# Performance work log

Measured on AMD Instinct MI355X. Metric: run time of the kernel, lower is better.

## Reference

```python
import jax, jax.numpy as jnp
import numpy as np

N, E, EL = 100000, 1600000, 200000
IN_FEATS, H, N_LAYERS = 128, 128, 3
HL = ((N_LAYERS + 1) * H) // 2  # PyG JK-LSTM hidden = (num_layers*channels)//2 = 256
EPS = 1e-5


def setup_inputs() -> dict:
    key = jax.random.key(0)
    ks = jax.random.split(key, 16)
    p = lambda k, shape: (jax.random.normal(k, shape, jnp.float32) * 0.05)
    return {
        "edge_index": jax.random.randint(ks[0], (2, E), 0, N),
        "x": jax.random.normal(ks[1], (N, IN_FEATS), jnp.float32),
        "edge_label_index": jax.random.randint(ks[2], (2, EL), 0, N),
        # GCNConv
        "gcn_w": p(ks[3], (IN_FEATS, H)), "gcn_b": jnp.zeros((H,), jnp.float32),
        # SGConv stack (lin applied AFTER propagation, K=1)
        "sg_w": p(ks[4], (N_LAYERS, H, H)), "sg_b": jnp.zeros((N_LAYERS, H), jnp.float32),
        # shared BatchNorm used between conv layers
        "bn_gamma": jnp.ones((H,), jnp.float32), "bn_beta": jnp.zeros((H,), jnp.float32),
        # bidirectional LSTM for JumpingKnowledge (torch gate order i,f,g,o)
        "w_ih_f": p(ks[5], (4 * HL, H)), "w_hh_f": p(ks[6], (4 * HL, HL)),
        "b_ih_f": jnp.zeros((4 * HL,), jnp.float32), "b_hh_f": jnp.zeros((4 * HL,), jnp.float32),
        "w_ih_b": p(ks[7], (4 * HL, H)), "w_hh_b": p(ks[8], (4 * HL, HL)),
        "b_ih_b": jnp.zeros((4 * HL,), jnp.float32), "b_hh_b": jnp.zeros((4 * HL,), jnp.float32),
        "att_w": p(ks[9], (2 * HL, 1)), "att_b": jnp.zeros((1,), jnp.float32),
        # edge predictor MLP
        "pred1_w": p(ks[10], (2 * H, H)), "pred1_b": jnp.zeros((H,), jnp.float32),
        "pbn_gamma": jnp.ones((H,), jnp.float32), "pbn_beta": jnp.zeros((H,), jnp.float32),
        "pred2_w": p(ks[11], (H, 1)), "pred2_b": jnp.zeros((1,), jnp.float32),
    }


def gcn_prop(x, src, dst, n):
    deg = jnp.zeros((n,), x.dtype).at[dst].add(jnp.ones((src.shape[0],), x.dtype)) + 1.0
    dinv = jax.lax.rsqrt(deg)
    norm = dinv[src] * dinv[dst]  # [E]
    out = jnp.zeros_like(x).at[dst].add(norm[:, None] * x[src])
    return out + (dinv * dinv)[:, None] * x  # self-loop contribution


def batchnorm(h, g, b):
    mu = h.mean(axis=0)
    var = ((h - mu) ** 2).mean(axis=0)
    return (h - mu) * jax.lax.rsqrt(var + EPS) * g + b


def lstm_dir(xs, w_ih, w_hh, b_ih, b_hh):
    # xs: [L, N, C] -> hidden states [L, N, HL]
    n = xs.shape[1]
    hh = w_hh.shape[1]
    def step(carry, xt):
        h, c = carry
        gates = xt @ w_ih.T + h @ w_hh.T + b_ih + b_hh
        i, f, g, o = jnp.split(gates, 4, axis=-1)
        c = jax.nn.sigmoid(f) * c + jax.nn.sigmoid(i) * jnp.tanh(g)
        h = jax.nn.sigmoid(o) * jnp.tanh(c)
        return (h, c), h
    init = (jnp.zeros((n, hh), xs.dtype), jnp.zeros((n, hh), xs.dtype))
    _, hs = jax.lax.scan(step, init, xs)
    return hs


def reference(edge_index, x, edge_label_index, gcn_w, gcn_b, sg_w, sg_b,
              bn_gamma, bn_beta, w_ih_f, w_hh_f, b_ih_f, b_hh_f,
              w_ih_b, w_hh_b, b_ih_b, b_hh_b, att_w, att_b,
              pred1_w, pred1_b, pbn_gamma, pbn_beta, pred2_w, pred2_b):
    src, dst = edge_index[0], edge_index[1]
    n = x.shape[0]
    hs = []
    # GCNConv: linear transform, then normalized propagation, then bias
    h = gcn_prop(x @ gcn_w, src, dst, n) + gcn_b
    h = batchnorm(jax.nn.relu(h), bn_gamma, bn_beta)  # dropout = identity (eval)
    hs.append(h)
    # SGConv (K=1): propagate then linear; last layer has no act/norm
    for i in range(N_LAYERS):
        h = gcn_prop(h, src, dst, n) @ sg_w[i] + sg_b[i]
        if i < N_LAYERS - 1:
            h = batchnorm(jax.nn.relu(h), bn_gamma, bn_beta)
        hs.append(h)
    xs = jnp.stack(hs, axis=0)  # [L, N, H]
    hf = lstm_dir(xs, w_ih_f, w_hh_f, b_ih_f, b_hh_f)
    hb = lstm_dir(xs[::-1], w_ih_b, w_hh_b, b_ih_b, b_hh_b)[::-1]
    seq = jnp.concatenate([hf, hb], axis=-1)  # [L, N, 2*HL]
    alpha = jax.nn.softmax((seq @ att_w)[..., 0] + att_b[0], axis=0)  # softmax over layers
    jk = jnp.einsum('lnh,ln->nh', xs, alpha)  # [N, H]
    # edge-level predictor
    row, col = edge_label_index[0], edge_label_index[1]
    z = jnp.concatenate([jk[row], jk[col]], axis=-1)  # [EL, 2H]
    z = jax.nn.relu(z @ pred1_w + pred1_b)
    z = batchnorm(z, pbn_gamma, pbn_beta)  # dropout = identity (eval)
    z = z @ pred2_w + pred2_b
    return jax.nn.sigmoid(z)
```

## Files before the change

### kernel.cpp

```cpp
#include <hip/hip_runtime.h>
#include <cstdint>

#define CDIV(a,b) (((a)+(b)-1)/(b))

typedef __bf16 bf16x8 __attribute__((ext_vector_type(8)));
typedef float  f32x4  __attribute__((ext_vector_type(4)));

__device__ __forceinline__ float bf2f(unsigned short u) {
    unsigned v = ((unsigned)u) << 16;
    float f; __builtin_memcpy(&f, &v, 4); return f;
}
__device__ __forceinline__ unsigned short f2bf(float f) {
    unsigned u; __builtin_memcpy(&u, &f, 4);
    u += 0x7fffu + ((u >> 16) & 1u);
    return (unsigned short)(u >> 16);
}
__device__ __forceinline__ float fsig(float x) { return 1.f / (1.f + __expf(-x)); }
__device__ __forceinline__ float ftanh(float x) { return 2.f * fsig(2.f * x) - 1.f; }

__device__ __forceinline__ void gld_lds16(const void* g, void* l) {
    __builtin_amdgcn_global_load_lds((__attribute__((address_space(1))) void*)(g),
                                     (__attribute__((address_space(3))) void*)(l), 16, 0, 0);
}


__global__ __launch_bounds__(256) void k_zero4(uint4* p, size_t n4) {
    size_t i = (size_t)blockIdx.x * 256 + threadIdx.x;
    if (i < n4) p[i] = make_uint4(0, 0, 0, 0);
}

__global__ __launch_bounds__(256) void k_deg(const int* ei, int* degi, int E) {
    int e = blockIdx.x * 256 + threadIdx.x;
    if (e < E) atomicAdd(&degi[ei[E + e]], 1);
}

__global__ __launch_bounds__(256) void k_dinv(const int* degi, float* dinv, int N) {
    int n = blockIdx.x * 256 + threadIdx.x;
    if (n < N) dinv[n] = rsqrtf((float)degi[n] + 1.f);
}

#define SCAN_B 2048
__global__ __launch_bounds__(256) void k_scan1(const int* in, int* out, int* bsum, int n) {
    __shared__ int ls[256];
    int b = blockIdx.x, t = threadIdx.x;
    int base = b * SCAN_B + t * 8;
    int v[8]; int s = 0;
#pragma unroll
    for (int i = 0; i < 8; ++i) { int idx = base + i; v[i] = (idx < n) ? in[idx] : 0; s += v[i]; }
    ls[t] = s; __syncthreads();
    for (int off = 1; off < 256; off <<= 1) {
        int x = (t >= off) ? ls[t - off] : 0;
        __syncthreads();
        ls[t] += x;
        __syncthreads();
    }
    int ex = ls[t] - s;
    if (t == 255) bsum[b] = ls[255];
    int run = ex;
#pragma unroll
    for (int i = 0; i < 8; ++i) { int idx = base + i; if (idx < n) out[idx] = run; run += v[i]; }
}
__global__ void k_scan2(int* bsum, int nb) {
    if (threadIdx.x == 0) {
        int acc = 0;
        for (int b = 0; b < nb; ++b) { int v = bsum[b]; bsum[b] = acc; acc += v; }
    }
}
__global__ __launch_bounds__(256) void k_scan3(int* rowp, int* curs, const int* bsum, int n) {
    int i = blockIdx.x * 256 + threadIdx.x;
    if (i < n) { int v = rowp[i] + bsum[i / SCAN_B]; rowp[i] = v; curs[i] = v; }
}
__global__ __launch_bounds__(256) void k_fill(const int* ei, int* curs, int* csr, int E) {
    int e = blockIdx.x * 256 + threadIdx.x;
    if (e < E) { int d = ei[E + e]; int pos = atomicAdd(&curs[d], 1); csr[pos] = ei[e]; }
}

__global__ __launch_bounds__(256) void k_xconv(const float* x, unsigned short* xb, int N, int Npad) {
    int idx = blockIdx.x * 256 + threadIdx.x;
    if (idx >= Npad * 64) return;
    int n = idx >> 6, q = idx & 63;
    ushort2 o;
    if (n < N) {
        float2 v = *(const float2*)&x[(size_t)n * 128 + q * 2];
        o = make_ushort2(f2bf(v.x), f2bf(v.y));
    } else o = make_ushort2(0, 0);
    *(ushort2*)&xb[(size_t)n * 128 + q * 2] = o;
}

__global__ __launch_bounds__(256) void k_packT(const float* W, unsigned short* BT, int K, int Nout) {
    int idx = blockIdx.x * 256 + threadIdx.x;
    if (idx >= K * Nout) return;
    int o = idx / K, k = idx % K;
    BT[idx] = f2bf(W[(size_t)k * Nout + o]);
}

__global__ __launch_bounds__(256) void k_packlstm4(const float* wih, const float* whh, unsigned short* BT) {
    int idx = blockIdx.x * 256 + threadIdx.x;
    if (idx >= 1024 * 384) return;
    int e = idx & 7, u = idx >> 3;
    int l4 = u & 3, l15 = (u >> 2) & 15, ni = (u >> 6) & 1;
    int rest = u >> 7;
    int ks = rest % 12, G = rest / 12;
    int gate = ni * 2 + (l15 >> 3);
    int hid = G * 8 + (l15 & 7);
    int srow = gate * 256 + hid;
    int k = ks * 32 + l4 * 8 + e;
    float v = (k < 128) ? wih[(size_t)srow * 128 + k] : whh[(size_t)srow * 256 + (k - 128)];
    BT[idx] = f2bf(v);
}
__global__ __launch_bounds__(256) void k_packbias4(const float* bih, const float* bhh, float* bias) {
    int c = blockIdx.x * 256 + threadIdx.x;
    if (c >= 1024) return;
    int G = c >> 5, cc = c & 31;
    int ni = cc >> 4, ll = cc & 15;
    int gate = ni * 2 + (ll >> 3);
    int hid = G * 8 + (ll & 7);
    int srow = gate * 256 + hid;
    bias[c] = bih[srow] + bhh[srow];
}


__global__ __launch_bounds__(256) void k_prop(const unsigned short* __restrict__ X,
                                              const int* __restrict__ rowp, const int* __restrict__ cnt,
                                              const int* __restrict__ csr, const float* __restrict__ dinv,
                                              const float* __restrict__ bias, int relu,
                                              int N, int Npad, unsigned short* __restrict__ OUT) {
    int node = (blockIdx.x * 256 + threadIdx.x) >> 4;
    if (node >= Npad) return;
    const int g = threadIdx.x & 15;
    unsigned short* op = OUT + (size_t)node * 128 + g * 8;
    if (node >= N) { *(uint4*)op = make_uint4(0, 0, 0, 0); return; }
    const int beg = rowp[node], num = cnt[node];
    const float di = dinv[node];
    float a[8];
#pragma unroll
    for (int j = 0; j < 8; ++j) a[j] = 0.f;
    if (num > 0) {
        int s = csr[beg];
        float ws = dinv[s];
        uint4 q = *(const uint4*)&X[(size_t)s * 128 + g * 8];
        for (int i = 0; i < num; ++i) {
            int sn = (i + 1 < num) ? csr[beg + i + 1] : s;
            float wn = dinv[sn];
            uint4 qn = *(const uint4*)&X[(size_t)sn * 128 + g * 8];
            unsigned q0 = q.x, q1 = q.y, q2 = q.z, q3 = q.w;
            a[0] = fmaf(ws, bf2f((unsigned short)(q0 & 0xffffu)), a[0]);
            a[1] = fmaf(ws, bf2f((unsigned short)(q0 >> 16)), a[1]);
            a[2] = fmaf(ws, bf2f((unsigned short)(q1 & 0xffffu)), a[2]);
            a[3] = fmaf(ws, bf2f((unsigned short)(q1 >> 16)), a[3]);
            a[4] = fmaf(ws, bf2f((unsigned short)(q2 & 0xffffu)), a[4]);
            a[5] = fmaf(ws, bf2f((unsigned short)(q2 >> 16)), a[5]);
            a[6] = fmaf(ws, bf2f((unsigned short)(q3 & 0xffffu)), a[6]);
            a[7] = fmaf(ws, bf2f((unsigned short)(q3 >> 16)), a[7]);
            s = sn; ws = wn; q = qn;
        }
    }
    uint4 xq = *(const uint4*)&X[(size_t)node * 128 + g * 8];
    unsigned x0 = xq.x, x1 = xq.y, x2 = xq.z, x3 = xq.w;
    const float dd = di * di;
    float o0 = di * a[0] + dd * bf2f((unsigned short)(x0 & 0xffffu));
    float o1 = di * a[1] + dd * bf2f((unsigned short)(x0 >> 16));
    float o2 = di * a[2] + dd * bf2f((unsigned short)(x1 & 0xffffu));
    float o3 = di * a[3] + dd * bf2f((unsigned short)(x1 >> 16));
    float o4 = di * a[4] + dd * bf2f((unsigned short)(x2 & 0xffffu));
    float o5 = di * a[5] + dd * bf2f((unsigned short)(x2 >> 16));
    float o6 = di * a[6] + dd * bf2f((unsigned short)(x3 & 0xffffu));
    float o7 = di * a[7] + dd * bf2f((unsigned short)(x3 >> 16));
    if (bias) {
        const float* bp = bias + g * 8;
        o0 += bp[0]; o1 += bp[1]; o2 += bp[2]; o3 += bp[3];
        o4 += bp[4]; o5 += bp[5]; o6 += bp[6]; o7 += bp[7];
    }
    if (relu) {
        o0 = fmaxf(o0, 0.f); o1 = fmaxf(o1, 0.f); o2 = fmaxf(o2, 0.f); o3 = fmaxf(o3, 0.f);
        o4 = fmaxf(o4, 0.f); o5 = fmaxf(o5, 0.f); o6 = fmaxf(o6, 0.f); o7 = fmaxf(o7, 0.f);
    }
    uint4 r;
    r.x = (unsigned)f2bf(o0) | ((unsigned)f2bf(o1) << 16);
    r.y = (unsigned)f2bf(o2) | ((unsigned)f2bf(o3) << 16);
    r.z = (unsigned)f2bf(o4) | ((unsigned)f2bf(o5) << 16);
    r.w = (unsigned)f2bf(o6) | ((unsigned)f2bf(o7) << 16);
    *(uint4*)op = r;
}


__global__ __launch_bounds__(256) void k_stats(const unsigned short* __restrict__ X, int rows, float* part) {
    __shared__ float ls[512];
    int t = threadIdx.x, b = blockIdx.x;
    int ch = t & 127, half = t >> 7;
    float s = 0.f, s2 = 0.f;
    for (int r = b * 2 + half; r < rows; r += 512) {
        float v = bf2f(X[(size_t)r * 128 + ch]);
        s += v; s2 += v * v;
    }
    ls[t] = s; ls[256 + t] = s2;
    __syncthreads();
    if (t < 128) {
        part[b * 256 + t] = ls[t] + ls[t + 128];
        part[b * 256 + 128 + t] = ls[256 + t] + ls[256 + t + 128];
    }
}
__global__ void k_bnfinal(const float* part, int nb, float rows,
                          const float* gamma, const float* beta, float* bnst) {
    int ch = threadIdx.x;
    if (ch >= 128) return;
    float s = 0.f, s2 = 0.f;
    for (int b = 0; b < nb; ++b) { s += part[b * 256 + ch]; s2 += part[b * 256 + 128 + ch]; }
    float mu = s / rows, var = s2 / rows - mu * mu;
    float sc = gamma[ch] * rsqrtf(var + 1e-5f);
    bnst[ch] = sc;
    bnst[128 + ch] = beta[ch] - mu * sc;
}
__global__ __launch_bounds__(256) void k_apply(const unsigned short* in, const float* bnst,
                                               unsigned short* outv, int N, int Npad) {
    int idx = blockIdx.x * 256 + threadIdx.x;
    if (idx >= Npad * 64) return;
    int n = idx >> 6, q = idx & 63;
    ushort2 o;
    if (n < N) {
        ushort2 v = *(const ushort2*)&in[(size_t)n * 128 + q * 2];
        int c0 = q * 2;
        o = make_ushort2(f2bf(bf2f(v.x) * bnst[c0] + bnst[128 + c0]),
                         f2bf(bf2f(v.y) * bnst[c0 + 1] + bnst[128 + c0 + 1]));
    } else o = make_ushort2(0, 0);
    *(ushort2*)&outv[(size_t)n * 128 + q * 2] = o;
}


template<int GATHER>
__device__ __forceinline__ void gemm_core(
    const unsigned short* __restrict__ A0, int lda0, int K0,
    const unsigned short* __restrict__ A1, int lda1, int Ktot,
    const unsigned short* __restrict__ BT, int ldb,
    const int* __restrict__ gR, const int* __restrict__ gC, int ELr,
    int m0, int c0, unsigned short* sA, unsigned short* sB, f32x4 acc[4][4]) {
    const int tid = threadIdx.x;
    const int wid = tid >> 6, lane = tid & 63;
    const int l15 = lane & 15, l4 = lane >> 4;
    const int wr = (wid >> 1) * 64, wc = (wid & 1) * 64;
    const int crow = lane >> 3;
    const int cslot = (lane & 7) ^ crow;
    const int nK = Ktot >> 6;
    for (int ks = 0; ks < nK; ++ks) {
        const int k0 = ks << 6;
#pragma unroll
        for (int i = 0; i < 4; ++i) {
            const int chunk = wid * 4 + i;
            const int row = chunk * 8 + crow;
            const unsigned short* bs = BT + (size_t)(c0 + row) * ldb + k0 + (cslot << 3);
            gld_lds16(bs, sB + chunk * 512);
            if constexpr (GATHER) {
                int e = m0 + row; if (e >= ELr) e = ELr - 1;
                const int nid = (k0 < K0) ? gR[e] : gC[e];
                const unsigned short* as = A0 + (size_t)nid * lda0 + (k0 & (K0 - 1)) + (lane & 7) * 8;
                *(uint4*)(sA + chunk * 512 + crow * 64 + (((lane & 7) ^ crow) << 3)) = *(const uint4*)as;
            } else {
                const unsigned short* as = (k0 < K0)
                    ? A0 + (size_t)(m0 + row) * lda0 + k0 + (cslot << 3)
                    : A1 + (size_t)(m0 + row) * lda1 + (k0 - K0) + (cslot << 3);
                gld_lds16(as, sA + chunk * 512);
            }
        }
        __syncthreads();
#pragma unroll
        for (int kk = 0; kk < 2; ++kk) {
            const int c8 = kk * 4 + l4;
            const int rs = l15 & 7;
            bf16x8 av[4], bv[4];
#pragma unroll
            for (int i = 0; i < 4; ++i)
                av[i] = *(const bf16x8*)(sA + (wr + i * 16 + l15) * 64 + ((c8 ^ rs) << 3));
#pragma unroll
            for (int i = 0; i < 4; ++i)
                bv[i] = *(const bf16x8*)(sB + (wc + i * 16 + l15) * 64 + ((c8 ^ rs) << 3));
#pragma unroll
            for (int mi = 0; mi < 4; ++mi)
#pragma unroll
                for (int ni = 0; ni < 4; ++ni)
                    acc[mi][ni] = __builtin_amdgcn_mfma_f32_16x16x32_bf16(av[mi], bv[ni], acc[mi][ni], 0, 0, 0);
        }
        __syncthreads();
    }
}

template<int GATHER>
__global__ __launch_bounds__(256) void k_gemm(
    const unsigned short* __restrict__ A0, int lda0, int K0,
    const unsigned short* __restrict__ A1, int lda1, int Ktot,
    const unsigned short* __restrict__ BT, int ldb,
    const int* __restrict__ gR, const int* __restrict__ gC, int ELr,
    const float* __restrict__ bias, int relu,
    unsigned short* __restrict__ C, int ldc, int NT) {
    extern __shared__ char smem[];
    unsigned short* sA = (unsigned short*)smem;
    unsigned short* sB = (unsigned short*)(smem + 16384);
    int mt = blockIdx.x / NT, nt = blockIdx.x % NT;
    int m0 = mt * 128, c0 = nt * 128;
    f32x4 acc[4][4];
#pragma unroll
    for (int a = 0; a < 4; ++a)
#pragma unroll
        for (int b = 0; b < 4; ++b) acc[a][b] = (f32x4){0.f, 0.f, 0.f, 0.f};
    gemm_core<GATHER>(A0, lda0, K0, A1, lda1, Ktot, BT, ldb, gR, gC, ELr, m0, c0, sA, sB, acc);
    const int tid = threadIdx.x;
    const int wid = tid >> 6, lane = tid & 63;
    const int l15 = lane & 15, l4 = lane >> 4;
    const int wr = (wid >> 1) * 64, wc = (wid & 1) * 64;
#pragma unroll
    for (int ni = 0; ni < 4; ++ni) {
        int col = c0 + wc + ni * 16 + l15;
        float bv = bias ? bias[col] : 0.f;
#pragma unroll
        for (int mi = 0; mi < 4; ++mi) {
            int rbase = m0 + wr + mi * 16 + l4 * 4;
#pragma unroll
            for (int j = 0; j < 4; ++j) {
                float v = acc[mi][ni][j] + bv;
                if (relu) v = fmaxf(v, 0.f);
                C[(size_t)(rbase + j) * ldc + col] = f2bf(v);
            }
        }
    }
}


__global__ __launch_bounds__(1024)
void k_lstm_fused(
    const unsigned short* __restrict__ xs,
    const unsigned short* __restrict__ BT2f, const unsigned short* __restrict__ BT2b,
    const float* __restrict__ bias2f, const float* __restrict__ bias2b,
    const float* __restrict__ att_w,
    float* __restrict__ scores,
    int N, int Npad) {
    __shared__ unsigned short xls[64 * 128];
    __shared__ unsigned short hbuf[2][64 * 256];
    __shared__ float c_ld[64 * 256];
    __shared__ float sc_ld[16][64];

    const int tid = threadIdx.x;
    const int wid = tid >> 6, lane = tid & 63;
    const int l15 = lane & 15, l4 = lane >> 4;
    const int rs = l15 & 7;
    const int m0 = blockIdx.x * 64;
    const int loff = (l15 * 4 + l4) * 8;
    const bool hi = (l15 & 8) != 0;

    float scl[4] = {0.f, 0.f, 0.f, 0.f};

#pragma unroll 1
    for (int dir = 0; dir < 2; ++dir) {
        const unsigned short* BT2 = dir ? BT2b : BT2f;
        const float* bias2 = dir ? bias2b : bias2f;
        const float* attw = att_w + dir * 256;
        for (int i = tid; i < 2048; i += 1024) ((uint4*)hbuf[0])[i] = make_uint4(0, 0, 0, 0);
        for (int i = tid; i < 4096; i += 1024) ((uint4*)c_ld)[i] = make_uint4(0, 0, 0, 0);
        __syncthreads();
        unsigned short* hcur = hbuf[0];
        unsigned short* hnxt = hbuf[1];

#pragma unroll 1
        for (int t = 0; t < 4; ++t) {
            const int lyr = dir ? (3 - t) : t;
            if (wid < 8) {
                const unsigned short* xl = xs + (size_t)lyr * Npad * 128;
#pragma unroll
                for (int i = 0; i < 2; ++i) {
                    int chunk = wid * 2 + i;
                    int row = chunk * 4 + l4;
                    gld_lds16(xl + (size_t)(m0 + row) * 128 + ((l15 ^ (row & 7)) << 3),
                              xls + chunk * 512);
                }
            }
            __syncthreads();

            float scA[4], scB[4];
#pragma unroll
            for (int a = 0; a < 4; ++a) { scA[a] = 0.f; scB[a] = 0.f; }

#pragma unroll 1
            for (int p = 0; p < 2; ++p) {
                const int G = wid * 2 + p;
                f32x4 acc[4][2];
#pragma unroll
                for (int a = 0; a < 4; ++a) {
                    acc[a][0] = (f32x4){0.f, 0.f, 0.f, 0.f};
                    acc[a][1] = (f32x4){0.f, 0.f, 0.f, 0.f};
                }
                const unsigned short* bp = BT2 + (size_t)G * 12288 + loff;
                bf16x8 f0a = *(const bf16x8*)(bp);
                bf16x8 f0b = *(const bf16x8*)(bp + 512);
                bf16x8 f1a = *(const bf16x8*)(bp + 1024);
                bf16x8 f1b = *(const bf16x8*)(bp + 1536);
#pragma unroll 1
                for (int ks = 0; ks < 4; ++ks) {
                    bf16x8 bv0 = f0a, bv1 = f0b;
                    f0a = f1a; f0b = f1b;
                    f1a = *(const bf16x8*)(bp + ((ks + 2) * 2 + 0) * 512);
                    f1b = *(const bf16x8*)(bp + ((ks + 2) * 2 + 1) * 512);
#pragma unroll
                    for (int mi = 0; mi < 4; ++mi) {
                        bf16x8 av = *(const bf16x8*)(xls + (mi * 16 + l15) * 128 +
                                                     (((ks * 4 + l4) ^ rs) << 3));
                        acc[mi][0] = __builtin_amdgcn_mfma_f32_16x16x32_bf16(av, bv0, acc[mi][0], 0, 0, 0);
                        acc[mi][1] = __builtin_amdgcn_mfma_f32_16x16x32_bf16(av, bv1, acc[mi][1], 0, 0, 0);
                    }
                }
#pragma unroll 1
                for (int ks = 4; ks < 12; ++ks) {
                    bf16x8 bv0 = f0a, bv1 = f0b;
                    f0a = f1a; f0b = f1b;
                    f1a = *(const bf16x8*)(bp + ((ks + 2) * 2 + 0) * 512);
                    f1b = *(const bf16x8*)(bp + ((ks + 2) * 2 + 1) * 512);
#pragma unroll
                    for (int mi = 0; mi < 4; ++mi) {
                        bf16x8 av = *(const bf16x8*)(hcur + (mi * 16 + l15) * 256 +
                                                     ((((ks - 4) * 4 + l4) ^ rs) << 3));
                        acc[mi][0] = __builtin_amdgcn_mfma_f32_16x16x32_bf16(av, bv0, acc[mi][0], 0, 0, 0);
                        acc[mi][1] = __builtin_amdgcn_mfma_f32_16x16x32_bf16(av, bv1, acc[mi][1], 0, 0, 0);
                    }
                }
                const float bi0 = bias2[G * 32 + l15];
                const float bi1 = bias2[G * 32 + 16 + l15];
                const float aw = attw[G * 8 + (l15 & 7)];
#pragma unroll
                for (int mi = 0; mi < 4; ++mi) {
                    float a00 = acc[mi][0][0] + bi0, a01 = acc[mi][0][1] + bi0;
                    float a02 = acc[mi][0][2] + bi0, a03 = acc[mi][0][3] + bi0;
                    float a10 = acc[mi][1][0] + bi1, a11 = acc[mi][1][1] + bi1;
                    float a12 = acc[mi][1][2] + bi1, a13 = acc[mi][1][3] + bi1;
                    float r0 = __shfl_xor(hi ? a00 : a02, 8);
                    float r1 = __shfl_xor(hi ? a01 : a03, 8);
                    float r2 = __shfl_xor(hi ? a10 : a12, 8);
                    float r3 = __shfl_xor(hi ? a11 : a13, 8);
                    float iA = hi ? r0  : a00,  fA = hi ? a02 : r0;
                    float gA = hi ? r2  : a10,  oA = hi ? a12 : r2;
                    float iB = hi ? r1  : a01,  fB = hi ? a03 : r1;
                    float gB = hi ? r3  : a11,  oB = hi ? a13 : r3;
                    const int rA = mi * 16 + l4 * 4 + (hi ? 2 : 0);
                    {
                        float gi = fsig(iA), gf = fsig(fA), gg = ftanh(gA), go = fsig(oA);
                        const int ca = rA * 256 + (((G ^ ((rA >> 2) & 7)) << 3) + (l15 & 7));
                        float cc = fmaf(gf, c_ld[ca], gi * gg);
                        c_ld[ca] = cc;
                        float hn = go * ftanh(cc);
                        scA[mi] = fmaf(hn, aw, scA[mi]);
                        *(unsigned short*)((char*)hnxt + rA * 512 +
                                           ((G ^ (rA & 7)) << 4) + (l15 & 7) * 2) = f2bf(hn);
                    }
                    {
                        const int rB = rA + 1;
                        float gi = fsig(iB), gf = fsig(fB), gg = ftanh(gB), go = fsig(oB);
                        const int cb = rB * 256 + (((G ^ ((rB >> 2) & 7)) << 3) + (l15 & 7));
                        float cc = fmaf(gf, c_ld[cb], gi * gg);
                        c_ld[cb] = cc;
                        float hn = go * ftanh(cc);
                        scB[mi] = fmaf(hn, aw, scB[mi]);
                        *(unsigned short*)((char*)hnxt + rB * 512 +
                                           ((G ^ (rB & 7)) << 4) + (l15 & 7) * 2) = f2bf(hn);
                    }
                }
            }
#pragma unroll
            for (int mi = 0; mi < 4; ++mi) {
                float sA = scA[mi], sB = scB[mi];
                sA += __shfl_xor(sA, 1); sA += __shfl_xor(sA, 2); sA += __shfl_xor(sA, 4);
                sB += __shfl_xor(sB, 1); sB += __shfl_xor(sB, 2); sB += __shfl_xor(sB, 4);
                if ((l15 & 7) == 0) {
                    int row = mi * 16 + l4 * 4 + (hi ? 2 : 0);
                    sc_ld[wid][row] = sA;
                    sc_ld[wid][row + 1] = sB;
                }
            }
            __syncthreads();
            if (tid < 64) {
                float s = 0.f;
#pragma unroll
                for (int w = 0; w < 16; ++w) s += sc_ld[w][tid];
#pragma unroll
                for (int l = 0; l < 4; ++l) scl[l] += (l == lyr) ? s : 0.f;
            }
            unsigned short* tmp = hcur; hcur = hnxt; hnxt = tmp;
        }
    }
    if (tid < 64) {
        int n = m0 + tid;
        if (n < N) {
#pragma unroll
            for (int l = 0; l < 4; ++l) scores[(size_t)l * N + n] = scl[l];
        }
    }
}


__global__ __launch_bounds__(256) void k_jk(const float* __restrict__ sc, const unsigned short* __restrict__ xs,
                                            unsigned short* __restrict__ jk, int N, int Npad) {
    int gw = (blockIdx.x * 256 + threadIdx.x) >> 6;
    if (gw >= N) return;
    int lane = threadIdx.x & 63;
    float s0 = sc[gw], s1 = sc[N + gw], s2 = sc[2 * N + gw], s3 = sc[3 * N + gw];
    float m = fmaxf(fmaxf(s0, s1), fmaxf(s2, s3));
    float e0 = __expf(s0 - m), e1 = __expf(s1 - m), e2 = __expf(s2 - m), e3 = __expf(s3 - m);
    float inv = 1.f / (e0 + e1 + e2 + e3);
    float a0 = e0 * inv, a1 = e1 * inv, a2 = e2 * inv, a3 = e3 * inv;
    size_t stride = (size_t)Npad * 128;
    const unsigned short* p = xs + (size_t)gw * 128 + lane * 2;
    ushort2 v0 = *(const ushort2*)p;
    ushort2 v1 = *(const ushort2*)(p + stride);
    ushort2 v2 = *(const ushort2*)(p + 2 * stride);
    ushort2 v3 = *(const ushort2*)(p + 3 * stride);
    float r0 = a0 * bf2f(v0.x) + a1 * bf2f(v1.x) + a2 * bf2f(v2.x) + a3 * bf2f(v3.x);
    float r1 = a0 * bf2f(v0.y) + a1 * bf2f(v1.y) + a2 * bf2f(v2.y) + a3 * bf2f(v3.y);
    *(ushort2*)&jk[(size_t)gw * 128 + lane * 2] = make_ushort2(f2bf(r0), f2bf(r1));
}

__global__ __launch_bounds__(256) void k_final(const unsigned short* __restrict__ z1, const float* __restrict__ bnst,
                                               const float* __restrict__ w2, const float* __restrict__ b2,
                                               float* __restrict__ out, int EL) {
    int e = (blockIdx.x * 256 + threadIdx.x) >> 6;
    if (e >= EL) return;
    int lane = threadIdx.x & 63;
    ushort2 z = *(const ushort2*)&z1[(size_t)e * 128 + lane * 2];
    int c0 = lane * 2;
    float y0 = bf2f(z.x) * bnst[c0] + bnst[128 + c0];
    float y1 = bf2f(z.y) * bnst[c0 + 1] + bnst[128 + c0 + 1];
    float p = y0 * w2[c0] + y1 * w2[c0 + 1];
#pragma unroll
    for (int off = 32; off; off >>= 1) p += __shfl_xor(p, off);
    if (lane == 0) out[e] = 1.f / (1.f + __expf(-(p + b2[0])));
}


extern "C" void kernel_launch(void* const* d_in, const int* in_sizes, int n_in,
                              void* d_out, int out_size, void* d_ws, size_t ws_size,
                              hipStream_t stream) {
    const int* ei      = (const int*)d_in[0];
    const float* x     = (const float*)d_in[1];
    const int* eli     = (const int*)d_in[2];
    const float* gcn_w = (const float*)d_in[3];
    const float* gcn_b = (const float*)d_in[4];
    const float* sg_w  = (const float*)d_in[5];
    const float* sg_b  = (const float*)d_in[6];
    const float* bn_g  = (const float*)d_in[7];
    const float* bn_b  = (const float*)d_in[8];
    const float* w_ih_f = (const float*)d_in[9];
    const float* w_hh_f = (const float*)d_in[10];
    const float* b_ih_f = (const float*)d_in[11];
    const float* b_hh_f = (const float*)d_in[12];
    const float* w_ih_b = (const float*)d_in[13];
    const float* w_hh_b = (const float*)d_in[14];
    const float* b_ih_b = (const float*)d_in[15];
    const float* b_hh_b = (const float*)d_in[16];
    const float* att_w = (const float*)d_in[17];
    const float* p1_w  = (const float*)d_in[19];
    const float* p1_b  = (const float*)d_in[20];
    const float* pbn_g = (const float*)d_in[21];
    const float* pbn_b = (const float*)d_in[22];
    const float* p2_w  = (const float*)d_in[23];
    const float* p2_b  = (const float*)d_in[24];

    const int E = in_sizes[0] / 2;
    const int N = in_sizes[1] / 128;
    const int EL = in_sizes[2] / 2;
    const int Npad = CDIV(N, 128) * 128;
    const int ELpad = CDIV(EL, 128) * 128;
    const size_t NB128 = (size_t)Npad * 128 * 2;

    char* wsp = (char*)d_ws;
    size_t off = 0;
    auto A = [&](size_t b) -> char* {
        char* p = wsp + off;
        off = (off + b + 255) & ~(size_t)255;
        return p;
    };
    int* degi = (int*)A((size_t)N * 4);
    float* dinv = (float*)A((size_t)N * 4);
    int* rowp = (int*)A((size_t)N * 4);
    int* curs = (int*)A((size_t)N * 4);
    int* bsum = (int*)A(256 * 4);
    unsigned short* gT   = (unsigned short*)A(128 * 128 * 2);
    unsigned short* sgT  = (unsigned short*)A(3 * 128 * 128 * 2);
    unsigned short* p1T  = (unsigned short*)A(128 * 256 * 2);
    unsigned short* BTf  = (unsigned short*)A(1024 * 384 * 2);
    unsigned short* BTb  = (unsigned short*)A(1024 * 384 * 2);
    float* biasf = (float*)A(1024 * 4);
    float* biasb = (float*)A(1024 * 4);
    float* part = (float*)A(256 * 256 * 4);
    float* bnst = (float*)A(256 * 4);
    float* scores = (float*)A((size_t)4 * N * 4);
    unsigned short* xs = (unsigned short*)A(NB128 * 4);
    const size_t arena0 = off;
    int* csr = (int*)A((size_t)E * 4);
    unsigned short* xb   = (unsigned short*)A(NB128);
    unsigned short* bufA = (unsigned short*)A(NB128);
    unsigned short* bufB = (unsigned short*)A(NB128);
    const size_t convEnd = off;
    off = arena0;
    unsigned short* jk = (unsigned short*)A((size_t)N * 128 * 2);
    unsigned short* z1 = (unsigned short*)A((size_t)ELpad * 128 * 2);
    const size_t predEnd = off;
    if (convEnd > ws_size || predEnd > ws_size) return;

    k_zero4<<<CDIV((size_t)N * 4, 16 * 256), 256, 0, stream>>>((uint4*)degi, CDIV((size_t)N * 4, 16));
    k_deg<<<CDIV(E, 256), 256, 0, stream>>>(ei, degi, E);
    k_dinv<<<CDIV(N, 256), 256, 0, stream>>>(degi, dinv, N);
    int nb = CDIV(N, SCAN_B);
    k_scan1<<<nb, 256, 0, stream>>>(degi, rowp, bsum, N);
    k_scan2<<<1, 64, 0, stream>>>(bsum, nb);
    k_scan3<<<CDIV(N, 256), 256, 0, stream>>>(rowp, curs, bsum, N);
    k_fill<<<CDIV(E, 256), 256, 0, stream>>>(ei, curs, csr, E);

    k_xconv<<<CDIV(Npad * 64, 256), 256, 0, stream>>>(x, xb, N, Npad);
    k_packT<<<CDIV(128 * 128, 256), 256, 0, stream>>>(gcn_w, gT, 128, 128);
    for (int i = 0; i < 3; ++i)
        k_packT<<<CDIV(128 * 128, 256), 256, 0, stream>>>(sg_w + (size_t)i * 128 * 128, sgT + (size_t)i * 128 * 128, 128, 128);
    k_packT<<<CDIV(256 * 128, 256), 256, 0, stream>>>(p1_w, p1T, 256, 128);
    k_packlstm4<<<CDIV(1024 * 384, 256), 256, 0, stream>>>(w_ih_f, w_hh_f, BTf);
    k_packlstm4<<<CDIV(1024 * 384, 256), 256, 0, stream>>>(w_ih_b, w_hh_b, BTb);
    k_packbias4<<<4, 256, 0, stream>>>(b_ih_f, b_hh_f, biasf);
    k_packbias4<<<4, 256, 0, stream>>>(b_ih_b, b_hh_b, biasb);

    const int MT = Npad / 128;
    k_gemm<0><<<MT, 256, 32768, stream>>>(xb, 128, 128, nullptr, 0, 128, gT, 128,
                                          nullptr, nullptr, 0, nullptr, 0, bufA, 128, 1);
    k_prop<<<CDIV(Npad * 16, 256), 256, 0, stream>>>(bufA, rowp, degi, csr, dinv, gcn_b, 1, N, Npad, bufB);
    k_stats<<<256, 256, 0, stream>>>(bufB, N, part);
    k_bnfinal<<<1, 128, 0, stream>>>(part, 256, (float)N, bn_g, bn_b, bnst);
    k_apply<<<CDIV(Npad * 64, 256), 256, 0, stream>>>(bufB, bnst, xs, N, Npad);

    for (int i = 0; i < 3; ++i) {
        k_prop<<<CDIV(Npad * 16, 256), 256, 0, stream>>>(xs + (size_t)i * Npad * 128, rowp, degi, csr, dinv,
                                                         nullptr, 0, N, Npad, bufA);
        unsigned short* dst = (i < 2) ? bufB : xs + (size_t)3 * Npad * 128;
        k_gemm<0><<<MT, 256, 32768, stream>>>(bufA, 128, 128, nullptr, 0, 128,
                                              sgT + (size_t)i * 128 * 128, 128,
                                              nullptr, nullptr, 0, sg_b + i * 128, (i < 2) ? 1 : 0, dst, 128, 1);
        if (i < 2) {
            k_stats<<<256, 256, 0, stream>>>(bufB, N, part);
            k_bnfinal<<<1, 128, 0, stream>>>(part, 256, (float)N, bn_g, bn_b, bnst);
            k_apply<<<CDIV(Npad * 64, 256), 256, 0, stream>>>(bufB, bnst, xs + (size_t)(i + 1) * Npad * 128, N, Npad);
        }
    }

    k_lstm_fused<<<Npad / 64, 1024, 0, stream>>>(xs, BTf, BTb, biasf, biasb, att_w, scores, N, Npad);

    k_jk<<<CDIV(N * 64, 256), 256, 0, stream>>>(scores, xs, jk, N, Npad);

    const int MTe = ELpad / 128;
    k_gemm<1><<<MTe, 256, 32768, stream>>>(jk, 128, 128, nullptr, 0, 256, p1T, 256,
                                           eli, eli + EL, EL, p1_b, 1, z1, 128, 1);
    k_stats<<<256, 256, 0, stream>>>(z1, EL, part);
    k_bnfinal<<<1, 128, 0, stream>>>(part, 256, (float)EL, pbn_g, pbn_b, bnst);
    k_final<<<CDIV(EL * 64, 256), 256, 0, stream>>>(z1, bnst, p2_w, p2_b, (float*)d_out, EL);
    (void)n_in; (void)out_size;
}
```

Before: 2.546 ms.

## Keep LSTM cell state in registers and halve LSTM block to 512 threads

The fused LSTM kernel now runs 8 waves per block, each handling four gate groups instead of two, and keeps the cell state in per-thread registers rather than a 64KB shared-memory array. The score-reduction scratch is aliased onto the x tile buffer, so shared memory per block drops from about 112KB to about 80KB, which may let more blocks share a CU. The intent is to cut LDS traffic for the cell state and raise occupancy. In exchange each wave does twice the serial work, register pressure rises, the B-operand prefetch pipelining is removed, and an extra barrier is added per timestep.

```diff
diff --git a/kernel.cpp b/kernel.cpp
--- a/kernel.cpp
+++ b/kernel.cpp
@@ -324,7 +324,7 @@
 }
 
 
-__global__ __launch_bounds__(1024)
+__global__ __launch_bounds__(512)
 void k_lstm_fused(
     const unsigned short* __restrict__ xs,
     const unsigned short* __restrict__ BT2f, const unsigned short* __restrict__ BT2b,
@@ -332,10 +332,10 @@
     const float* __restrict__ att_w,
     float* __restrict__ scores,
     int N, int Npad) {
-    __shared__ unsigned short xls[64 * 128];
+    __shared__ char shx[64 * 128 * 2];
     __shared__ unsigned short hbuf[2][64 * 256];
-    __shared__ float c_ld[64 * 256];
-    __shared__ float sc_ld[16][64];
+    unsigned short* xls = (unsigned short*)shx;
+    float* sc_ld = (float*)shx;
 
     const int tid = threadIdx.x;
     const int wid = tid >> 6, lane = tid & 63;
@@ -352,16 +352,21 @@
         const unsigned short* BT2 = dir ? BT2b : BT2f;
         const float* bias2 = dir ? bias2b : bias2f;
         const float* attw = att_w + dir * 256;
-        for (int i = tid; i < 2048; i += 1024) ((uint4*)hbuf[0])[i] = make_uint4(0, 0, 0, 0);
-        for (int i = tid; i < 4096; i += 1024) ((uint4*)c_ld)[i] = make_uint4(0, 0, 0, 0);
+        for (int i = tid; i < 2048; i += 512) ((uint4*)hbuf[0])[i] = make_uint4(0, 0, 0, 0);
         __syncthreads();
         unsigned short* hcur = hbuf[0];
         unsigned short* hnxt = hbuf[1];
+        float c0[4][2], c1[4][2], c2[4][2], c3[4][2];
+#pragma unroll
+        for (int a = 0; a < 4; ++a) {
+            c0[a][0] = 0.f; c0[a][1] = 0.f; c1[a][0] = 0.f; c1[a][1] = 0.f;
+            c2[a][0] = 0.f; c2[a][1] = 0.f; c3[a][0] = 0.f; c3[a][1] = 0.f;
+        }
 
 #pragma unroll 1
         for (int t = 0; t < 4; ++t) {
             const int lyr = dir ? (3 - t) : t;
-            if (wid < 8) {
+            {
                 const unsigned short* xl = xs + (size_t)lyr * Npad * 128;
 #pragma unroll
                 for (int i = 0; i < 2; ++i) {
@@ -377,89 +382,87 @@
 #pragma unroll
             for (int a = 0; a < 4; ++a) { scA[a] = 0.f; scB[a] = 0.f; }
 
-#pragma unroll 1
-            for (int p = 0; p < 2; ++p) {
-                const int G = wid * 2 + p;
-                f32x4 acc[4][2];
-#pragma unroll
-                for (int a = 0; a < 4; ++a) {
-                    acc[a][0] = (f32x4){0.f, 0.f, 0.f, 0.f};
-                    acc[a][1] = (f32x4){0.f, 0.f, 0.f, 0.f};
-                }
-                const unsigned short* bp = BT2 + (size_t)G * 12288 + loff;
-                bf16x8 f0a = *(const bf16x8*)(bp);
-                bf16x8 f0b = *(const bf16x8*)(bp + 512);
-                bf16x8 f1a = *(const bf16x8*)(bp + 1024);
-                bf16x8 f1b = *(const bf16x8*)(bp + 1536);
-#pragma unroll 1
-                for (int ks = 0; ks < 4; ++ks) {
-                    bf16x8 bv0 = f0a, bv1 = f0b;
-                    f0a = f1a; f0b = f1b;
-                    f1a = *(const bf16x8*)(bp + ((ks + 2) * 2 + 0) * 512);
-                    f1b = *(const bf16x8*)(bp + ((ks + 2) * 2 + 1) * 512);
-#pragma unroll
-                    for (int mi = 0; mi < 4; ++mi) {
-                        bf16x8 av = *(const bf16x8*)(xls + (mi * 16 + l15) * 128 +
-                                                     (((ks * 4 + l4) ^ rs) << 3));
-                        acc[mi][0] = __builtin_amdgcn_mfma_f32_16x16x32_bf16(av, bv0, acc[mi][0], 0, 0, 0);
-                        acc[mi][1] = __builtin_amdgcn_mfma_f32_16x16x32_bf16(av, bv1, acc[mi][1], 0, 0, 0);
-                    }
-                }
-#pragma unroll 1
-                for (int ks = 4; ks < 12; ++ks) {
-                    bf16x8 bv0 = f0a, bv1 = f0b;
-                    f0a = f1a; f0b = f1b;
-                    f1a = *(const bf16x8*)(bp + ((ks + 2) * 2 + 0) * 512);
-                    f1b = *(const bf16x8*)(bp + ((ks + 2) * 2 + 1) * 512);
-#pragma unroll
-                    for (int mi = 0; mi < 4; ++mi) {
-                        bf16x8 av = *(const bf16x8*)(hcur + (mi * 16 + l15) * 256 +
-                                                     ((((ks - 4) * 4 + l4) ^ rs) << 3));
-                        acc[mi][0] = __builtin_amdgcn_mfma_f32_16x16x32_bf16(av, bv0, acc[mi][0], 0, 0, 0);
-                        acc[mi][1] = __builtin_amdgcn_mfma_f32_16x16x32_bf16(av, bv1, acc[mi][1], 0, 0, 0);
-                    }
-                }
-                const float bi0 = bias2[G * 32 + l15];
-                const float bi1 = bias2[G * 32 + 16 + l15];
-                const float aw = attw[G * 8 + (l15 & 7)];
-#pragma unroll
-                for (int mi = 0; mi < 4; ++mi) {
-                    float a00 = acc[mi][0][0] + bi0, a01 = acc[mi][0][1] + bi0;
-                    float a02 = acc[mi][0][2] + bi0, a03 = acc[mi][0][3] + bi0;
-                    float a10 = acc[mi][1][0] + bi1, a11 = acc[mi][1][1] + bi1;
-                    float a12 = acc[mi][1][2] + bi1, a13 = acc[mi][1][3] + bi1;
-                    float r0 = __shfl_xor(hi ? a00 : a02, 8);
-                    float r1 = __shfl_xor(hi ? a01 : a03, 8);
-                    float r2 = __shfl_xor(hi ? a10 : a12, 8);
-                    float r3 = __shfl_xor(hi ? a11 : a13, 8);
-                    float iA = hi ? r0  : a00,  fA = hi ? a02 : r0;
-                    float gA = hi ? r2  : a10,  oA = hi ? a12 : r2;
-                    float iB = hi ? r1  : a01,  fB = hi ? a03 : r1;
-                    float gB = hi ? r3  : a11,  oB = hi ? a13 : r3;
-                    const int rA = mi * 16 + l4 * 4 + (hi ? 2 : 0);
-                    {
-                        float gi = fsig(iA), gf = fsig(fA), gg = ftanh(gA), go = fsig(oA);
-                        const int ca = rA * 256 + (((G ^ ((rA >> 2) & 7)) << 3) + (l15 & 7));
-                        float cc = fmaf(gf, c_ld[ca], gi * gg);
-                        c_ld[ca] = cc;
-                        float hn = go * ftanh(cc);
-                        scA[mi] = fmaf(hn, aw, scA[mi]);
-                        *(unsigned short*)((char*)hnxt + rA * 512 +
-                                           ((G ^ (rA & 7)) << 4) + (l15 & 7) * 2) = f2bf(hn);
-                    }
-                    {
-                        const int rB = rA + 1;
-                        float gi = fsig(iB), gf = fsig(fB), gg = ftanh(gB), go = fsig(oB);
-                        const int cb = rB * 256 + (((G ^ ((rB >> 2) & 7)) << 3) + (l15 & 7));
-                        float cc = fmaf(gf, c_ld[cb], gi * gg);
-                        c_ld[cb] = cc;
-                        float hn = go * ftanh(cc);
-                        scB[mi] = fmaf(hn, aw, scB[mi]);
-                        *(unsigned short*)((char*)hnxt + rB * 512 +
-                                           ((G ^ (rB & 7)) << 4) + (l15 & 7) * 2) = f2bf(hn);
-                    }
-                }
+#define DO_PASS(P, cp)                                                               \
+            {                                                                        \
+                const int G = wid * 4 + (P);                                         \
+                f32x4 acc[4][2];                                                     \
+                _Pragma("unroll")                                                    \
+                for (int a = 0; a < 4; ++a) {                                        \
+                    acc[a][0] = (f32x4){0.f, 0.f, 0.f, 0.f};                         \
+                    acc[a][1] = (f32x4){0.f, 0.f, 0.f, 0.f};                         \
+                }                                                                    \
+                const unsigned short* bpp = BT2 + (size_t)G * 12288 + loff;          \
+                _Pragma("unroll 1")                                                  \
+                for (int ks = 0; ks < 4; ++ks) {                                     \
+                    bf16x8 bv0 = *(const bf16x8*)(bpp + (ks * 2 + 0) * 512);         \
+                    bf16x8 bv1 = *(const bf16x8*)(bpp + (ks * 2 + 1) * 512);         \
+                    _Pragma("unroll")                                                \
+                    for (int mi = 0; mi < 4; ++mi) {                                 \
+                        bf16x8 av = *(const bf16x8*)(xls + (mi * 16 + l15) * 128 +   \
+                                                     (((ks * 4 + l4) ^ rs) << 3));   \
+                        acc[mi][0] = __builtin_amdgcn_mfma_f32_16x16x32_bf16(av, bv0, acc[mi][0], 0, 0, 0); \
+                        acc[mi][1] = __builtin_amdgcn_mfma_f32_16x16x32_bf16(av, bv1, acc[mi][1], 0, 0, 0); \
+                    }                                                                \
+                }                                                                    \
+                _Pragma("unroll 1")                                                  \
+                for (int ks = 4; ks < 12; ++ks) {                                    \
+                    bf16x8 bv0 = *(const bf16x8*)(bpp + (ks * 2 + 0) * 512);         \
+                    bf16x8 bv1 = *(const bf16x8*)(bpp + (ks * 2 + 1) * 512);         \
+                    _Pragma("unroll")                                                \
+                    for (int mi = 0; mi < 4; ++mi) {                                 \
+                        bf16x8 av = *(const bf16x8*)(hcur + (mi * 16 + l15) * 256 +  \
+                                                     ((((ks - 4) * 4 + l4) ^ rs) << 3)); \
+                        acc[mi][0] = __builtin_amdgcn_mfma_f32_16x16x32_bf16(av, bv0, acc[mi][0], 0, 0, 0); \
+                        acc[mi][1] = __builtin_amdgcn_mfma_f32_16x16x32_bf16(av, bv1, acc[mi][1], 0, 0, 0); \
+                    }                                                                \
+                }                                                                    \
+                const float bi0 = bias2[G * 32 + l15];                               \
+                const float bi1 = bias2[G * 32 + 16 + l15];                          \
+                const float aw = attw[G * 8 + (l15 & 7)];                            \
+                _Pragma("unroll")                                                    \
+                for (int mi = 0; mi < 4; ++mi) {                                     \
+                    float a00 = acc[mi][0][0] + bi0, a01 = acc[mi][0][1] + bi0;      \
+                    float a02 = acc[mi][0][2] + bi0, a03 = acc[mi][0][3] + bi0;      \
+                    float a10 = acc[mi][1][0] + bi1, a11 = acc[mi][1][1] + bi1;      \
+                    float a12 = acc[mi][1][2] + bi1, a13 = acc[mi][1][3] + bi1;      \
+                    float r0 = __shfl_xor(hi ? a00 : a02, 8);                        \
+                    float r1 = __shfl_xor(hi ? a01 : a03, 8);                        \
+                    float r2 = __shfl_xor(hi ? a10 : a12, 8);                        \
+                    float r3 = __shfl_xor(hi ? a11 : a13, 8);                        \
+                    float iA = hi ? r0  : a00,  fA = hi ? a02 : r0;                  \
+                    float gA = hi ? r2  : a10,  oA = hi ? a12 : r2;                  \
+                    float iB = hi ? r1  : a01,  fB = hi ? a03 : r1;                  \
+                    float gB = hi ? r3  : a11,  oB = hi ? a13 : r3;                  \
+                    const int rA = mi * 16 + l4 * 4 + (hi ? 2 : 0);                  \
+                    {                                                                \
+                        float gi = fsig(iA), gf = fsig(fA), gg = ftanh(gA), go = fsig(oA); \
+                        float cc = fmaf(gf, cp[mi][0], gi * gg);                     \
+                        cp[mi][0] = cc;                                              \
+                        float hn = go * ftanh(cc);                                   \
+                        scA[mi] = fmaf(hn, aw, scA[mi]);                             \
+                        *(unsigned short*)((char*)hnxt + rA * 512 +                  \
+                                           ((G ^ (rA & 7)) << 4) + (l15 & 7) * 2) = f2bf(hn); \
+                    }                                                                \
+                    {                                                                \
+                        const int rB = rA + 1;                                       \
+                        float gi = fsig(iB), gf = fsig(fB), gg = ftanh(gB), go = fsig(oB); \
+                        float cc = fmaf(gf, cp[mi][1], gi * gg);                     \
+                        cp[mi][1] = cc;                                              \
+                        float hn = go * ftanh(cc);                                   \
+                        scB[mi] = fmaf(hn, aw, scB[mi]);                             \
+                        *(unsigned short*)((char*)hnxt + rB * 512 +                  \
+                                           ((G ^ (rB & 7)) << 4) + (l15 & 7) * 2) = f2bf(hn); \
+                    }                                                                \
+                }                                                                    \
             }
+
+            DO_PASS(0, c0)
+            DO_PASS(1, c1)
+            DO_PASS(2, c2)
+            DO_PASS(3, c3)
+#undef DO_PASS
+
+            __syncthreads();
 #pragma unroll
             for (int mi = 0; mi < 4; ++mi) {
                 float sA = scA[mi], sB = scB[mi];
@@ -467,18 +470,19 @@
                 sB += __shfl_xor(sB, 1); sB += __shfl_xor(sB, 2); sB += __shfl_xor(sB, 4);
                 if ((l15 & 7) == 0) {
                     int row = mi * 16 + l4 * 4 + (hi ? 2 : 0);
-                    sc_ld[wid][row] = sA;
-                    sc_ld[wid][row + 1] = sB;
+                    sc_ld[wid * 64 + row] = sA;
+                    sc_ld[wid * 64 + row + 1] = sB;
                 }
             }
             __syncthreads();
             if (tid < 64) {
                 float s = 0.f;
 #pragma unroll
-                for (int w = 0; w < 16; ++w) s += sc_ld[w][tid];
+                for (int w = 0; w < 8; ++w) s += sc_ld[w * 64 + tid];
 #pragma unroll
                 for (int l = 0; l < 4; ++l) scl[l] += (l == lyr) ? s : 0.f;
             }
+            __syncthreads();
             unsigned short* tmp = hcur; hcur = hnxt; hnxt = tmp;
         }
     }
@@ -641,7 +645,7 @@
         }
     }
 
-    k_lstm_fused<<<Npad / 64, 1024, 0, stream>>>(xs, BTf, BTb, biasf, biasb, att_w, scores, N, Npad);
+    k_lstm_fused<<<Npad / 64, 512, 0, stream>>>(xs, BTf, BTb, biasf, biasb, att_w, scores, N, Npad);
 
     k_jk<<<CDIV(N * 64, 256), 256, 0, stream>>>(scores, xs, jk, N, Npad);
 
```

New measurement: 2.444 ms. 1.04x faster.
